# Kernel optimization log

Measured on AMD Instinct MI355X. Metric: run time of the kernel, lower is better.

Reference implementation:

```python
import jax, jax.numpy as jnp
import numpy as np

EMBED = 1024
B, S = 8, 2048

def setup_inputs() -> dict:
    key = jax.random.key(0)
    k1, k2 = jax.random.split(key)
    x = jax.random.normal(k1, (B, S, EMBED), dtype=jnp.float32)
    # torch Linear(embed, 3*embed): store weight already transposed as [E, 3E]
    W_qkv = jax.random.normal(k2, (EMBED, 3 * EMBED), dtype=jnp.float32) * (1.0 / np.sqrt(EMBED))
    b_qkv = jnp.zeros((3 * EMBED,), dtype=jnp.float32)
    return {"x": x, "W_qkv": W_qkv, "b_qkv": b_qkv}

def reference(x, W_qkv, b_qkv):
    E = x.shape[-1]
    qkv = x @ W_qkv + b_qkv                      # [B,S,3E]
    Q, K, V = jnp.split(qkv, 3, axis=-1)         # each [B,S,E]
    scale = 1.0 / jnp.sqrt(jnp.asarray(E, x.dtype))
    scores = jnp.einsum('bqe,bke->bqk', Q, K) * scale  # [B,S,S]
    attn = jax.nn.softmax(scores, axis=-1)
    return jnp.einsum('bqk,bke->bqe', attn, V)   # [B,S,E]
```

## Files before the change

kernel.cpp:

```cpp
#include <hip/hip_runtime.h>

typedef unsigned short u16;
typedef unsigned int u32;
typedef __attribute__((ext_vector_type(8))) short short8;
typedef __attribute__((ext_vector_type(4))) short short4v;
typedef __attribute__((ext_vector_type(4))) float f32x4;

__device__ __forceinline__ u16 f2bf(float f) {
    u32 u = __float_as_uint(f);
    u32 r = (u + 0x7fffu + ((u >> 16) & 1u)) >> 16;
    return (u16)r;
}
__device__ __forceinline__ float bf2f(u16 h) {
    return __uint_as_float(((u32)h) << 16);
}

__device__ __forceinline__ void gload_lds16(const void* g, void* l) {
    __builtin_amdgcn_global_load_lds((const __attribute__((address_space(1))) void*)g,
                                     (__attribute__((address_space(3))) void*)l, 16, 0, 0);
}

#define BARRIER() do { __builtin_amdgcn_sched_barrier(0); __builtin_amdgcn_s_barrier(); __builtin_amdgcn_sched_barrier(0); } while (0)
#define VMCNT(N)  asm volatile("s_waitcnt vmcnt(" #N ")" ::: "memory")

#define STAGE(ptr, LDG, LOFF, RBASE, kelem) \
    do { gload_lds16((ptr) + (size_t)(RBASE) * (LDG) + (kelem),        lds + (LOFF) + ((RBASE) + (wid << 3)) * 128); \
         gload_lds16((ptr) + (size_t)((RBASE) + 64) * (LDG) + (kelem), lds + (LOFF) + ((RBASE) + 64 + (wid << 3)) * 128); } while (0)

template<int ROFF, int QH>
__device__ __forceinline__ void ld_a(short8 (&a)[4][2], const char* lds, int arow, int c0, int c1) {
    #pragma unroll
    for (int mf = 0; mf < 4; ++mf) {
        a[mf][0] = *(const short8*)(lds + ROFF + QH * 16384 + mf * 2048 + arow + c0);
        a[mf][1] = *(const short8*)(lds + ROFF + QH * 16384 + mf * 2048 + arow + c1);
    }
}
template<int ROFF, int QH>
__device__ __forceinline__ void ld_b(short8 (&b)[2][2], const char* lds, int brow, int c0, int c1) {
    #pragma unroll
    for (int nf = 0; nf < 2; ++nf) {
        b[nf][0] = *(const short8*)(lds + ROFF + QH * 16384 + nf * 2048 + brow + c0);
        b[nf][1] = *(const short8*)(lds + ROFF + QH * 16384 + nf * 2048 + brow + c1);
    }
}

template<int QM, int QN>
__device__ __forceinline__ void mfq(f32x4 (&acc)[2][4][2][2], short8 (&a)[4][2], short8 (&b)[2][2]) {
    __builtin_amdgcn_s_setprio(1);
    #pragma unroll
    for (int mf = 0; mf < 4; ++mf)
        #pragma unroll
        for (int nf = 0; nf < 2; ++nf) {
            acc[QM][mf][QN][nf] = __builtin_amdgcn_mfma_f32_16x16x32_bf16(a[mf][0], b[nf][0], acc[QM][mf][QN][nf], 0, 0, 0);
            acc[QM][mf][QN][nf] = __builtin_amdgcn_mfma_f32_16x16x32_bf16(a[mf][1], b[nf][1], acc[QM][mf][QN][nf], 0, 0, 0);
        }
    __builtin_amdgcn_s_setprio(0);
}

template<int EPI, int LDA, int LDB, int LDC, int K>
__global__ __launch_bounds__(512, 2)
void gemm8p(const u16* __restrict__ A, long long sA,
            const u16* __restrict__ B, long long sB,
            void* __restrict__ Cv, long long sC,
            const float* __restrict__ bias, float scale,
            int GX, int GY)
{
    extern __shared__ char lds[];
    const int tid  = threadIdx.x;
    const int wid  = tid >> 6;
    const int lane = tid & 63;

    const int nwg = gridDim.x;
    int bid = blockIdx.x;
    bid = (bid & 7) * (nwg >> 3) + (bid >> 3);
    const int bx  = bid % GX;
    const int rem = bid / GX;
    const int by  = rem % GY;
    const long long z = rem / GY;

    const int bm = by * 256, bn = bx * 256;
    const u16* Atile = A + z * sA + (size_t)bm * LDA;
    const u16* Btile = B + z * sB + (size_t)bn * LDB;

    const int wm = wid >> 2, wn = wid & 3;
    const int l15   = lane & 15;
    const int lxor  = (lane & 7) << 4;
    const int khi   = (lane >> 4) << 4;
    const int colk0 = khi ^ lxor;
    const int colk1 = (64 + khi) ^ lxor;
    const int arow  = (wm * 64 + l15) * 128;
    const int brow  = (wn * 32 + l15) * 128;

    const int swz = ((lane & 7) ^ (lane >> 3)) << 3;
    const u16* pA = Atile + (size_t)((wid << 3) + (lane >> 3)) * LDA + swz;
    const u16* pB = Btile + (size_t)((wid << 3) + (lane >> 3)) * LDB + swz;

    f32x4 acc[2][4][2][2];
    #pragma unroll
    for (int i = 0; i < 2; ++i)
        #pragma unroll
        for (int m = 0; m < 4; ++m)
            #pragma unroll
            for (int j = 0; j < 2; ++j)
                #pragma unroll
                for (int n = 0; n < 2; ++n)
                    acc[i][m][j][n] = (f32x4){0.f, 0.f, 0.f, 0.f};

    STAGE(pA, LDA, 0,     0,   0);  STAGE(pA, LDA, 0,     128, 0);
    STAGE(pB, LDB, 32768, 0,   0);  STAGE(pB, LDB, 32768, 128, 0);
    STAGE(pA, LDA, 65536, 0,   64);
    STAGE(pB, LDB, 98304, 0,   64); STAGE(pB, LDB, 98304, 128, 64);
    VMCNT(6);
    BARRIER();

    short8 a[4][2], b0[2][2], b1[2][2];
    const int NI = K >> 7;

    for (int it = 0; it < NI; ++it) {
        const bool more = (it + 1 < NI);
        const int kc1 = it * 128 + 64;
        const int kn  = it * 128 + 128;
        const int kn2 = kn + 64;

        VMCNT(6);
        ld_a<0, 0>(a, lds, arow, colk0, colk1);
        ld_b<32768, 0>(b0, lds, brow, colk0, colk1);
        STAGE(pA, LDA, 65536, 128, kc1);
        BARRIER(); mfq<0, 0>(acc, a, b0);
        ld_b<32768, 1>(b1, lds, brow, colk0, colk1);
        BARRIER(); mfq<0, 1>(acc, a, b1);
        ld_a<0, 1>(a, lds, arow, colk0, colk1);
        if (more) STAGE(pB, LDB, 32768, 0, kn);
        BARRIER(); mfq<1, 1>(acc, a, b1);
        if (more) STAGE(pB, LDB, 32768, 128, kn);
        BARRIER(); mfq<1, 0>(acc, a, b0);
        if (more) { VMCNT(4); } else { VMCNT(0); }
        ld_a<65536, 0>(a, lds, arow, colk0, colk1);
        ld_b<98304, 0>(b0, lds, brow, colk0, colk1);
        if (more) STAGE(pA, LDA, 0, 0, kn);
        BARRIER(); mfq<0, 0>(acc, a, b0);
        ld_b<98304, 1>(b1, lds, brow, colk0, colk1);
        if (more) STAGE(pA, LDA, 0, 128, kn);
        BARRIER(); mfq<0, 1>(acc, a, b1);
        ld_a<65536, 1>(a, lds, arow, colk0, colk1);
        if (more) { STAGE(pB, LDB, 98304, 0, kn2); STAGE(pB, LDB, 98304, 128, kn2); }
        BARRIER(); mfq<1, 1>(acc, a, b1);
        if (more) STAGE(pA, LDA, 65536, 0, kn2);
        BARRIER(); mfq<1, 0>(acc, a, b0);
    }

    const int r0 = (lane >> 4) * 4;
    const int cc = lane & 15;
    #pragma unroll
    for (int qn = 0; qn < 2; ++qn)
        #pragma unroll
        for (int nf = 0; nf < 2; ++nf) {
            const int col = bn + qn * 128 + wn * 32 + nf * 16 + cc;
            const float badd = (EPI == 0) ? bias[col] : 0.f;
            #pragma unroll
            for (int qm = 0; qm < 2; ++qm)
                #pragma unroll
                for (int mf = 0; mf < 4; ++mf) {
                    const int row = bm + qm * 128 + wm * 64 + mf * 16 + r0;
                    #pragma unroll
                    for (int r = 0; r < 4; ++r) {
                        const float v = acc[qm][mf][qn][nf][r] * scale + badd;
                        if (EPI == 2) ((float*)Cv + z * sC)[(size_t)(row + r) * LDC + col] = v;
                        else          ((u16*)Cv + z * sC)[(size_t)(row + r) * LDC + col] = f2bf(v);
                    }
                }
        }
}

__global__ __launch_bounds__(256)
void cvt_f32_bf16(const float* __restrict__ in, u16* __restrict__ out, int n8)
{
    const int i = blockIdx.x * 256 + threadIdx.x;
    if (i >= n8) return;
    const float4* p = (const float4*)in;
    const float4 a = p[2 * i], b = p[2 * i + 1];
    short8 o;
    o[0] = (short)f2bf(a.x); o[1] = (short)f2bf(a.y);
    o[2] = (short)f2bf(a.z); o[3] = (short)f2bf(a.w);
    o[4] = (short)f2bf(b.x); o[5] = (short)f2bf(b.y);
    o[6] = (short)f2bf(b.z); o[7] = (short)f2bf(b.w);
    ((short8*)out)[i] = o;
}

__global__ __launch_bounds__(256)
void cvt_w_t(const float* __restrict__ W, u16* __restrict__ Wt)
{
    __shared__ u16 T[32][33];
    const int tid = threadIdx.x;
    const int tr = tid >> 3;
    const int tc = (tid & 7) * 4;
    const int c0 = blockIdx.x * 32;
    const int r0 = blockIdx.y * 32;
    const float4 v = *(const float4*)&W[(size_t)(r0 + tr) * 3072 + c0 + tc];
    T[tr][tc + 0] = f2bf(v.x); T[tr][tc + 1] = f2bf(v.y);
    T[tr][tc + 2] = f2bf(v.z); T[tr][tc + 3] = f2bf(v.w);
    __syncthreads();
    short4v o;
    o[0] = (short)T[tc + 0][tr]; o[1] = (short)T[tc + 1][tr];
    o[2] = (short)T[tc + 2][tr]; o[3] = (short)T[tc + 3][tr];
    *(short4v*)&Wt[(size_t)(c0 + tr) * 1024 + r0 + tc] = o;
}

__global__ __launch_bounds__(256)
void trans_v(const u16* __restrict__ qkv, u16* __restrict__ Vt)
{
    __shared__ u16 T[32][33];
    const int tid = threadIdx.x;
    const int tr = tid >> 3;
    const int tc = (tid & 7) * 4;
    const int e0 = blockIdx.x * 32;
    const int s0 = blockIdx.y * 32;
    const int b  = blockIdx.z;
    const short4v v = *(const short4v*)&qkv[(size_t)(b * 2048 + s0 + tr) * 3072 + 2048 + e0 + tc];
    T[tr][tc + 0] = (u16)v[0]; T[tr][tc + 1] = (u16)v[1];
    T[tr][tc + 2] = (u16)v[2]; T[tr][tc + 3] = (u16)v[3];
    __syncthreads();
    short4v o;
    o[0] = (short)T[tc + 0][tr]; o[1] = (short)T[tc + 1][tr];
    o[2] = (short)T[tc + 2][tr]; o[3] = (short)T[tc + 3][tr];
    *(short4v*)&Vt[(size_t)b * 1024 * 2048 + (size_t)(e0 + tr) * 2048 + s0 + tc] = o;
}

__global__ __launch_bounds__(256)
void softmax_bf16(u16* __restrict__ S)
{
    u16* row = S + (size_t)blockIdx.x * 2048;
    const int tid  = threadIdx.x;
    const int wid  = tid >> 6;
    const int lane = tid & 63;
    __shared__ float red[4];

    const short8 v8 = *(const short8*)&row[tid * 8];
    float v[8];
    float m = -3.4e38f;
    #pragma unroll
    for (int j = 0; j < 8; ++j) { v[j] = bf2f((u16)v8[j]); m = fmaxf(m, v[j]); }
    #pragma unroll
    for (int off = 32; off; off >>= 1) m = fmaxf(m, __shfl_xor(m, off));
    if (lane == 0) red[wid] = m;
    __syncthreads();
    m = fmaxf(fmaxf(red[0], red[1]), fmaxf(red[2], red[3]));
    float s = 0.f;
    #pragma unroll
    for (int j = 0; j < 8; ++j) { v[j] = __expf(v[j] - m); s += v[j]; }
    #pragma unroll
    for (int off = 32; off; off >>= 1) s += __shfl_xor(s, off);
    __syncthreads();
    if (lane == 0) red[wid] = s;
    __syncthreads();
    s = red[0] + red[1] + red[2] + red[3];
    const float inv = 1.f / s;
    short8 o;
    #pragma unroll
    for (int j = 0; j < 8; ++j) o[j] = (short)f2bf(v[j] * inv);
    *(short8*)&row[tid * 8] = o;
}

extern "C" void kernel_launch(void* const* d_in, const int* in_sizes, int n_in,
                              void* d_out, int out_size, void* d_ws, size_t ws_size,
                              hipStream_t stream) {
    const float* x    = (const float*)d_in[0];
    const float* W    = (const float*)d_in[1];
    const float* bias = (const float*)d_in[2];
    float* out = (float*)d_out;

    const int B = 8, S = 2048, E = 1024, N3 = 3072;
    const int M = B * S;

    char* ws = (char*)d_ws;
    u16* xb   = (u16*)ws;
    u16* Wtb  = (u16*)(ws + 33554432);
    u16* qkvb = (u16*)(ws + 39845888);
    u16* Vtb  = (u16*)(ws + 140509184);
    u16* Sb   = (u16*)(ws + 174063616);

    const size_t need_full = 174063616ull + (size_t)B * S * S * 2;
    const bool full = ws_size >= need_full;
    const float sc = 1.0f / 32.0f;
    const int LDSB = 131072;

    auto kQKV = gemm8p<0, 1024, 1024, 3072, 1024>;
    auto kQKT = gemm8p<1, 3072, 3072, 2048, 1024>;
    auto kPV  = gemm8p<2, 2048, 2048, 1024, 2048>;
    (void)hipFuncSetAttribute(reinterpret_cast<const void*>(kQKV),
                              hipFuncAttributeMaxDynamicSharedMemorySize, LDSB);
    (void)hipFuncSetAttribute(reinterpret_cast<const void*>(kQKT),
                              hipFuncAttributeMaxDynamicSharedMemorySize, LDSB);
    (void)hipFuncSetAttribute(reinterpret_cast<const void*>(kPV),
                              hipFuncAttributeMaxDynamicSharedMemorySize, LDSB);

    cvt_f32_bf16<<<dim3((M * E) / 8 / 256), 256, 0, stream>>>(x, xb, (M * E) / 8);
    cvt_w_t<<<dim3(96, 32), 256, 0, stream>>>(W, Wtb);

    kQKV<<<dim3(12 * 64), 512, LDSB, stream>>>(xb, 0, Wtb, 0, qkvb, 0, bias, 1.0f, 12, 64);

    trans_v<<<dim3(32, 64, 8), 256, 0, stream>>>(qkvb, Vtb);

    if (full) {
        kQKT<<<dim3(8 * 8 * 8), 512, LDSB, stream>>>(
            qkvb, (long long)S * N3, qkvb + E, (long long)S * N3,
            Sb, (long long)S * S, nullptr, sc, 8, 8);
        softmax_bf16<<<dim3(B * S), 256, 0, stream>>>(Sb);
        kPV<<<dim3(4 * 8 * 8), 512, LDSB, stream>>>(
            Sb, (long long)S * S, Vtb, (long long)E * S,
            out, (long long)S * E, nullptr, 1.0f, 4, 8);
    } else {
        for (int b = 0; b < B; ++b) {
            const u16* Qb = qkvb + (size_t)b * S * N3;
            kQKT<<<dim3(8 * 8), 512, LDSB, stream>>>(
                Qb, 0, Qb + E, 0, Sb, 0, nullptr, sc, 8, 8);
            softmax_bf16<<<dim3(S), 256, 0, stream>>>(Sb);
            kPV<<<dim3(4 * 8), 512, LDSB, stream>>>(
                Sb, 0, Vtb + (size_t)b * E * S, 0,
                out + (size_t)b * S * E, 0, nullptr, 1.0f, 4, 8);
        }
    }
}
```

Baseline: 279.6 us.

## Double-buffer A fragments in registers and reschedule LDS loads in GEMM main loop

Splits the A register fragment into two buffers so the next A half can be read from LDS while MFMAs consume the current one. The first A load is hoisted before the loop and the next iteration's A is prefetched at the end of each iteration. Global-to-LDS staging and vmcnt waits are reordered to match. This raises VGPR usage and reshuffles the wait counts, which risks occupancy loss or a correctness hazard if a wait is placed too late.

```diff
diff --git a/kernel.cpp b/kernel.cpp
--- a/kernel.cpp
+++ b/kernel.cpp
@@ -113,7 +113,9 @@
     VMCNT(6);
     BARRIER();
 
-    short8 a[4][2], b0[2][2], b1[2][2];
+    short8 a0[4][2], a1[4][2], b0[2][2], b1[2][2];
+    ld_a<0, 0>(a0, lds, arow, colk0, colk1);
+
     const int NI = K >> 7;
 
     for (int it = 0; it < NI; ++it) {
@@ -123,30 +125,33 @@
         const int kn2 = kn + 64;
 
         VMCNT(6);
-        ld_a<0, 0>(a, lds, arow, colk0, colk1);
         ld_b<32768, 0>(b0, lds, brow, colk0, colk1);
         STAGE(pA, LDA, 65536, 128, kc1);
-        BARRIER(); mfq<0, 0>(acc, a, b0);
+        BARRIER(); mfq<0, 0>(acc, a0, b0);
         ld_b<32768, 1>(b1, lds, brow, colk0, colk1);
-        BARRIER(); mfq<0, 1>(acc, a, b1);
-        ld_a<0, 1>(a, lds, arow, colk0, colk1);
+        ld_a<0, 1>(a1, lds, arow, colk0, colk1);
         if (more) STAGE(pB, LDB, 32768, 0, kn);
-        BARRIER(); mfq<1, 1>(acc, a, b1);
+        BARRIER(); mfq<0, 1>(acc, a0, b1);
+        if (more) { VMCNT(4); } else { VMCNT(2); }
         if (more) STAGE(pB, LDB, 32768, 128, kn);
-        BARRIER(); mfq<1, 0>(acc, a, b0);
+        BARRIER(); mfq<1, 1>(acc, a1, b1);
+        ld_a<65536, 0>(a0, lds, arow, colk0, colk1);
+        if (more) STAGE(pA, LDA, 0, 0, kn);
+        BARRIER(); mfq<1, 0>(acc, a1, b0);
+        if (more) { VMCNT(6); } else { VMCNT(0); }
+        ld_b<98304, 0>(b0, lds, brow, colk0, colk1);
+        if (more) STAGE(pA, LDA, 0, 128, kn);
+        BARRIER(); mfq<0, 0>(acc, a0, b0);
+        ld_b<98304, 1>(b1, lds, brow, colk0, colk1);
+        ld_a<65536, 1>(a1, lds, arow, colk0, colk1);
+        if (more) STAGE(pB, LDB, 98304, 0, kn2);
+        BARRIER(); mfq<0, 1>(acc, a0, b1);
         if (more) { VMCNT(4); } else { VMCNT(0); }
-        ld_a<65536, 0>(a, lds, arow, colk0, colk1);
-        ld_b<98304, 0>(b0, lds, brow, colk0, colk1);
-        if (more) STAGE(pA, LDA, 0, 0, kn);
-        BARRIER(); mfq<0, 0>(acc, a, b0);
-        ld_b<98304, 1>(b1, lds, brow, colk0, colk1);
-        if (more) STAGE(pA, LDA, 0, 128, kn);
-        BARRIER(); mfq<0, 1>(acc, a, b1);
-        ld_a<65536, 1>(a, lds, arow, colk0, colk1);
-        if (more) { STAGE(pB, LDB, 98304, 0, kn2); STAGE(pB, LDB, 98304, 128, kn2); }
-        BARRIER(); mfq<1, 1>(acc, a, b1);
+        if (more) STAGE(pB, LDB, 98304, 128, kn2);
+        BARRIER(); mfq<1, 1>(acc, a1, b1);
+        if (more) ld_a<0, 0>(a0, lds, arow, colk0, colk1);
         if (more) STAGE(pA, LDA, 65536, 0, kn2);
-        BARRIER(); mfq<1, 0>(acc, a, b0);
+        BARRIER(); mfq<1, 0>(acc, a1, b0);
     }
 
     const int r0 = (lane >> 4) * 4;
```

Result: slower. 308.9 us (+10.5%).
